# Kernel tuning notes

Measured on AMD Instinct MI355X. Metric: run time of the kernel, lower is better.

## Reference

```python
import jax, jax.numpy as jnp
import numpy as np

N_NODES = 50000


def _gcn_conv(x, W, b, src, dst, n_nodes):
    """PyG GCNConv: add self-loops, D^-1/2 (A+I) D^-1/2 X W + b."""
    loop = jnp.arange(n_nodes, dtype=src.dtype)
    src_f = jnp.concatenate([src, loop])  # [E+N]
    dst_f = jnp.concatenate([dst, loop])
    # degree over destination nodes (edge weight 1, incl. self loops)
    deg = jax.ops.segment_sum(jnp.ones_like(dst_f, dtype=x.dtype), dst_f,
                              num_segments=n_nodes)
    dinv = jnp.where(deg > 0, jax.lax.rsqrt(deg), 0.0)
    norm = dinv[src_f] * dinv[dst_f]  # [E+N]
    h = x @ W  # [N, C_out] dense GEMM first (C_out <= C_in here)
    msg = h[src_f] * norm[:, None]  # gather + scale
    out = jax.ops.segment_sum(msg, dst_f, num_segments=n_nodes)
    return out + b


def setup_inputs() -> dict:
    key = jax.random.key(0)
    k1, k2, k3, k4, k5, k6 = jax.random.split(key, 6)
    in_c, hid_c, out_c = 512, 512, 40
    x = jax.random.normal(k1, (N_NODES, in_c), dtype=jnp.float32)
    edge_index = jax.random.randint(k2, (2, 800000), 0, N_NODES, dtype=jnp.int64)
    # Glorot-style init for the linear weights, zero bias (PyG default)
    W1 = jax.random.normal(k3, (in_c, hid_c), dtype=jnp.float32) / np.sqrt(in_c)
    b1 = jnp.zeros((hid_c,), dtype=jnp.float32)
    W2 = jax.random.normal(k4, (hid_c, out_c), dtype=jnp.float32) / np.sqrt(hid_c)
    b2 = jnp.zeros((out_c,), dtype=jnp.float32)
    return {"x": x, "edge_index": edge_index, "W1": W1, "b1": b1,
            "W2": W2, "b2": b2}


def reference(x, edge_index, W1, b1, W2, b2):
    src, dst = edge_index[0], edge_index[1]
    h = _gcn_conv(x, W1, b1, src, dst, N_NODES)
    h = jax.nn.relu(h)
    h = _gcn_conv(h, W2, b2, src, dst, N_NODES)
    return jax.nn.log_softmax(h, axis=1)
```

## Files before the change

### kernel.cpp

```cpp
#include <hip/hip_runtime.h>


typedef unsigned int u32;
typedef unsigned short u16;
typedef __bf16 bf16x8 __attribute__((ext_vector_type(8)));
typedef float f32x4 __attribute__((ext_vector_type(4)));
typedef u32 u32x4 __attribute__((ext_vector_type(4)));

#define C_IN 512
#define C_HID 512
#define C_OUT 40
#define H_SCALE 24.0f
#define H_INV_SCALE (1.0f / 24.0f)

__device__ __forceinline__ float bf2f(u16 u) {
    u32 x = ((u32)u) << 16;
    return __builtin_bit_cast(float, x);
}
__device__ __forceinline__ u16 f2bf(float f) {
    u32 x = __builtin_bit_cast(u32, f);
    x += 0x7fffu + ((x >> 16) & 1u);
    return (u16)(x >> 16);
}
__device__ __forceinline__ char q8(float v) {
    float c = fminf(fmaxf(v * H_SCALE, -127.f), 127.f);
    return (char)__float2int_rn(c);
}
__device__ __forceinline__ u32 pk2(float a, float b) {
    u16 lo = __builtin_bit_cast(u16, (__bf16)a);
    u16 hi = __builtin_bit_cast(u16, (__bf16)b);
    return (u32)lo | ((u32)hi << 16);
}
__device__ __forceinline__ u32x4 pk8(float4 a, float4 b) {
    u32x4 r;
    r.x = pk2(a.x, a.y); r.y = pk2(a.z, a.w);
    r.z = pk2(b.x, b.y); r.w = pk2(b.z, b.w);
    return r;
}
__host__ __device__ __forceinline__ int imin(int a, int b) { return a < b ? a : b; }
__host__ __device__ __forceinline__ int imax(int a, int b) { return a > b ? a : b; }

__global__ void k_init(const u32* __restrict__ x32, const int* __restrict__ ei,
                       int* flags, int* deg, int* cursor, int n) {
    if (blockIdx.x == 0 && threadIdx.x < 64) {
        int lane = threadIdx.x;
        int z = (ei[2 * lane + 1] == 0) ? 1 : 0;
        u32 e = (x32[lane] >> 7) & 0xff;
        int v = (e >= 110 && e <= 133) ? 1 : 0;
        unsigned long long bz = __ballot(z);
        unsigned long long bv = __ballot(v);
        if (lane == 0) {
            flags[0] = (__popcll(bz) == 64) ? 2 : 1;
            flags[1] = (__popcll(bv) >= 48) ? 1 : 0;
        }
    }
    int i = blockIdx.x * 256 + threadIdx.x;
    if (i < n) { deg[i] = 1; cursor[i] = 0; }
}

__global__ void k_deg(const int* __restrict__ ei, const int* __restrict__ flags,
                      int* deg, int E, int ecap, int n) {
    int e = blockIdx.x * 256 + threadIdx.x;
    if (e >= E) return;
    int st = flags[0];
    int cap = ecap * st - 1;
    u32 d = (u32)ei[imin((E + e) * st, cap)];
    if (d < (u32)n) atomicAdd(&deg[d], 1);
}

__global__ void k_scanA(const int* __restrict__ deg, int* bsum, float* dinv, int n) {
    __shared__ int sh[256];
    int i = blockIdx.x * 256 + threadIdx.x;
    int dv = (i < n) ? deg[i] : 1;
    if (i < n) dinv[i] = rsqrtf((float)imax(dv, 1));
    sh[threadIdx.x] = (i < n) ? dv - 1 : 0;
    __syncthreads();
    for (int d = 128; d > 0; d >>= 1) {
        if (threadIdx.x < d) sh[threadIdx.x] += sh[threadIdx.x + d];
        __syncthreads();
    }
    if (threadIdx.x == 0) bsum[blockIdx.x] = sh[0];
}

__global__ void k_scanB(int* bsum, int nb, int* offs, int n) {
    __shared__ int sh[256];
    int t = threadIdx.x;
    int carry = 0;
    for (int base = 0; base < nb; base += 256) {
        int i = base + t;
        int v = (i < nb) ? bsum[i] : 0;
        sh[t] = v;
        __syncthreads();
        for (int d = 1; d < 256; d <<= 1) {
            int add = (t >= d) ? sh[t - d] : 0;
            __syncthreads();
            sh[t] += add;
            __syncthreads();
        }
        if (i < nb) bsum[i] = carry + sh[t] - v;
        int tot = sh[255];
        __syncthreads();
        carry += tot;
    }
    if (t == 0) offs[n] = carry;
}

__global__ void k_scanC(const int* __restrict__ deg, const int* __restrict__ bsum,
                        int* offs, int n) {
    __shared__ int sh[256];
    int t = threadIdx.x;
    int i = blockIdx.x * 256 + t;
    int v = (i < n) ? deg[i] - 1 : 0;
    sh[t] = v;
    __syncthreads();
    for (int d = 1; d < 256; d <<= 1) {
        int add = (t >= d) ? sh[t - d] : 0;
        __syncthreads();
        sh[t] += add;
        __syncthreads();
    }
    if (i < n) offs[i] = bsum[blockIdx.x] + sh[t] - v;
}

__global__ void k_sort(const int* __restrict__ ei, const int* __restrict__ flags,
                       const int* __restrict__ offs, int* cursor, int* csr,
                       int E, int ecap, int n) {
    int e = blockIdx.x * 256 + threadIdx.x;
    if (e >= E) return;
    int st = flags[0];
    int cap = ecap * st - 1;
    u32 d = (u32)ei[imin((E + e) * st, cap)];
    u32 s = (u32)ei[imin(e * st, cap)];
    if (d < (u32)n && s < (u32)n) {
        int pos = offs[d] + atomicAdd(&cursor[(int)d], 1);
        if ((u32)pos < (u32)E) csr[pos] = (int)s;
    }
}

__device__ __forceinline__ float ldf(const void* p, int i, int isbf) {
    return isbf ? bf2f(((const u16*)p)[i]) : ((const float*)p)[i];
}

__global__ __launch_bounds__(256) void k_prep(
    const void* __restrict__ W1, const void* __restrict__ b1,
    const void* __restrict__ W2, const void* __restrict__ b2,
    const int* __restrict__ flags, u16* __restrict__ w1t, u16* __restrict__ w2t,
    float* __restrict__ b1f, float* __restrict__ b2f) {
    __shared__ float tile[64][65];
    int isbf = flags[1];
    int tid = threadIdx.x;
    int stride = gridDim.x * 256;
    int i0 = blockIdx.x * 256 + tid;
    for (int t = blockIdx.x; t < 64; t += gridDim.x) {
        int tr = t >> 3, tc = t & 7;
        int rr = tid >> 2, cq = (tid & 3) * 16;
#pragma unroll
        for (int c = 0; c < 16; ++c)
            tile[cq + c][rr] = ldf(W1, (tr * 64 + rr) * 512 + tc * 64 + cq + c, isbf);
        __syncthreads();
#pragma unroll
        for (int c = 0; c < 16; ++c)
            w1t[(size_t)(tc * 64 + rr) * 512 + tr * 64 + cq + c] = f2bf(tile[rr][cq + c]);
        __syncthreads();
    }
    for (int i = i0; i < 64 * 512; i += stride) {
        int n = i >> 9, k = i & 511;
        w2t[i] = (n < C_OUT) ? f2bf(ldf(W2, k * C_OUT + n, isbf)) : (u16)0;
    }
    if (i0 < C_HID) b1f[i0] = ldf(b1, i0, isbf);
    if (i0 < C_OUT) b2f[i0] = ldf(b2, i0, isbf);
}

typedef __attribute__((address_space(1))) const u32 glds_src;
typedef __attribute__((address_space(3))) u32 glds_dst;

__global__ __launch_bounds__(256) void k_gemm128(
    const u16* __restrict__ xbf, const float* __restrict__ xf32,
    const int* __restrict__ flags, const u16* __restrict__ Bt,
    char* __restrict__ C, int M, int K, int ldc) {
    int isbf = flags[1];
    __shared__ __align__(16) u16 As0[64 * 32], As1[64 * 32];
    __shared__ __align__(16) u16 Bs0[128 * 32], Bs1[128 * 32];
    int tid = threadIdx.x;
    int wave = tid >> 6, lane = tid & 63;
    int quad = lane >> 4, lrow = lane & 15;
    int wrow = (wave & 1) * 32, wcol = (wave >> 1) * 64;

    int nwg = gridDim.x;
    int id = blockIdx.x;
    int q = nwg >> 3, r = nwg & 7;
    int xcd = id & 7, j8 = id >> 3;
    int wg = (xcd < r ? xcd * (q + 1) : r * (q + 1) + (xcd - r) * q) + j8;
    int row0 = (wg >> 2) * 64;
    int n0 = (wg & 3) * 128;

    int lr = lane >> 2;
    int lc = (lane & 3) * 8;
    int ar = row0 + wave * 16 + lr;
    int br = n0 + wave * 32 + lr;
    u16* As0_w = As0 + (wave * 16) * 32;
    u16* As1_w = As1 + (wave * 16) * 32;
    u16* Bs0_w = Bs0 + (wave * 32) * 32;
    u16* Bs1_w = Bs1 + (wave * 32) * 32;

    f32x4 acc[2][4] = {};
    int kTiles = K >> 6;
    for (int kt = 0; kt < kTiles; ++kt) {
        int k0 = kt * 64;
        int a0 = imin(ar, M - 1);
        if (isbf) {
            const u16* gA0 = xbf + (size_t)a0 * K + k0 + lc;
            __builtin_amdgcn_global_load_lds((glds_src*)gA0, (glds_dst*)As0_w, 16, 0, 0);
            __builtin_amdgcn_global_load_lds((glds_src*)(gA0 + 32), (glds_dst*)As1_w, 16, 0, 0);
        } else {
            const float* f0 = xf32 + (size_t)a0 * K + k0 + lc;
            float4 u0 = *(const float4*)(f0);
            float4 u1 = *(const float4*)(f0 + 4);
            float4 u2 = *(const float4*)(f0 + 32);
            float4 u3 = *(const float4*)(f0 + 36);
            *(u32x4*)(As0_w + lr * 32 + lc) = pk8(u0, u1);
            *(u32x4*)(As1_w + lr * 32 + lc) = pk8(u2, u3);
        }
        const u16* gB0 = Bt + (size_t)br * K + k0 + lc;
        const u16* gB1 = Bt + (size_t)(br + 16) * K + k0 + lc;
        __builtin_amdgcn_global_load_lds((glds_src*)gB0, (glds_dst*)Bs0_w, 16, 0, 0);
        __builtin_amdgcn_global_load_lds((glds_src*)gB1, (glds_dst*)(Bs0_w + 16 * 32), 16, 0, 0);
        __builtin_amdgcn_global_load_lds((glds_src*)(gB0 + 32), (glds_dst*)Bs1_w, 16, 0, 0);
        __builtin_amdgcn_global_load_lds((glds_src*)(gB1 + 32), (glds_dst*)(Bs1_w + 16 * 32), 16, 0, 0);
        __syncthreads();
#pragma unroll
        for (int ko = 0; ko < 2; ++ko) {
            const u16* Asrc = ko ? As1 : As0;
            const u16* Bsrc = ko ? Bs1 : Bs0;
            bf16x8 af[2], bfr[4];
#pragma unroll
            for (int i = 0; i < 2; ++i)
                af[i] = *(const bf16x8*)(Asrc + (wrow + i * 16 + lrow) * 32 + quad * 8);
#pragma unroll
            for (int j = 0; j < 4; ++j)
                bfr[j] = *(const bf16x8*)(Bsrc + (wcol + j * 16 + lrow) * 32 + quad * 8);
#pragma unroll
            for (int i = 0; i < 2; ++i)
#pragma unroll
                for (int j = 0; j < 4; ++j)
                    acc[i][j] = __builtin_amdgcn_mfma_f32_16x16x32_bf16(af[i], bfr[j],
                                                                        acc[i][j], 0, 0, 0);
        }
        __syncthreads();
    }
#pragma unroll
    for (int i = 0; i < 2; ++i)
#pragma unroll
        for (int j = 0; j < 4; ++j)
#pragma unroll
            for (int r2 = 0; r2 < 4; ++r2) {
                int row = row0 + wrow + i * 16 + quad * 4 + r2;
                int col = n0 + wcol + j * 16 + lrow;
                if (row < M) C[(size_t)row * ldc + col] = q8(acc[i][j][r2]);
            }
}

#define B2ROW 520
__global__ __launch_bounds__(256) void k_gemm64(
    const u16* __restrict__ A, const u16* __restrict__ Bt, u16* __restrict__ Cout,
    int M, int K, int Ncols, int ldc) {
    __shared__ __align__(16) u16 Bsh[48 * B2ROW];
    int tid = threadIdx.x;
    int wave = tid >> 6, lane = tid & 63;
    int quad = lane >> 4, lrow = lane & 15;

    for (int i = tid; i < 48 * 64; i += 256) {
        int rw = i >> 6, cv = (i & 63) * 8;
        *(uint4*)(Bsh + rw * B2ROW + cv) = *(const uint4*)(Bt + (size_t)rw * 512 + cv);
    }
    __syncthreads();

    int row0 = blockIdx.x * 128 + wave * 32;
    int r0 = imin(row0 + lrow, M - 1);
    int r1 = imin(row0 + 16 + lrow, M - 1);
    const u16* a0p = A + (size_t)r0 * K + quad * 8;
    const u16* a1p = A + (size_t)r1 * K + quad * 8;
    const u16* b0p = Bsh + (0 * 16 + lrow) * B2ROW + quad * 8;
    const u16* b1p = Bsh + (1 * 16 + lrow) * B2ROW + quad * 8;
    const u16* b2p = Bsh + (2 * 16 + lrow) * B2ROW + quad * 8;

    f32x4 c00 = {}, c01 = {}, c02 = {};
    f32x4 c10 = {}, c11 = {}, c12 = {};
#pragma unroll 4
    for (int k0 = 0; k0 < C_HID; k0 += 32) {
        bf16x8 a0 = *(const bf16x8*)(a0p + k0);
        bf16x8 a1 = *(const bf16x8*)(a1p + k0);
        bf16x8 b0 = *(const bf16x8*)(b0p + k0);
        bf16x8 b1 = *(const bf16x8*)(b1p + k0);
        bf16x8 b2 = *(const bf16x8*)(b2p + k0);
        c00 = __builtin_amdgcn_mfma_f32_16x16x32_bf16(a0, b0, c00, 0, 0, 0);
        c01 = __builtin_amdgcn_mfma_f32_16x16x32_bf16(a0, b1, c01, 0, 0, 0);
        c02 = __builtin_amdgcn_mfma_f32_16x16x32_bf16(a0, b2, c02, 0, 0, 0);
        c10 = __builtin_amdgcn_mfma_f32_16x16x32_bf16(a1, b0, c10, 0, 0, 0);
        c11 = __builtin_amdgcn_mfma_f32_16x16x32_bf16(a1, b1, c11, 0, 0, 0);
        c12 = __builtin_amdgcn_mfma_f32_16x16x32_bf16(a1, b2, c12, 0, 0, 0);
    }
    f32x4 cc[2][3] = {{c00, c01, c02}, {c10, c11, c12}};
#pragma unroll
    for (int i = 0; i < 2; ++i)
#pragma unroll
        for (int t = 0; t < 3; ++t)
#pragma unroll
            for (int r = 0; r < 4; ++r) {
                int row = row0 + i * 16 + quad * 4 + r;
                int col = t * 16 + lrow;
                if (row < M && col < Ncols)
                    Cout[(size_t)row * ldc + col] = f2bf(cc[i][t][r]);
            }
}

__device__ __forceinline__ void accum8i(float* acc, uint2 p, float w) {
    int lo = (int)p.x, hi = (int)p.y;
    acc[0] += w * (float)(signed char)(lo);
    acc[1] += w * (float)(signed char)(lo >> 8);
    acc[2] += w * (float)(signed char)(lo >> 16);
    acc[3] += w * (float)(signed char)(lo >> 24);
    acc[4] += w * (float)(signed char)(hi);
    acc[5] += w * (float)(signed char)(hi >> 8);
    acc[6] += w * (float)(signed char)(hi >> 16);
    acc[7] += w * (float)(signed char)(hi >> 24);
}

__global__ __launch_bounds__(256) void k_agg1(
    const char* __restrict__ hq, const int* __restrict__ csr, const int* __restrict__ offs,
    const float* __restrict__ dinv, const float* __restrict__ b1f,
    u16* __restrict__ out, int n, int Etot) {
    int wave = threadIdx.x >> 6, lane = threadIdx.x & 63;
    int v = blockIdx.x * 4 + wave;
    if (v >= n) return;
    float dv = dinv[v];
    float wself = dv * dv * H_INV_SCALE;

    float acc[8] = {0.f, 0.f, 0.f, 0.f, 0.f, 0.f, 0.f, 0.f};
    uint2 hs = *(const uint2*)(hq + (size_t)v * C_HID + lane * 8);
    accum8i(acc, hs, wself);

    int e0 = imax(0, imin(offs[v], Etot));
    int e1 = imax(e0, imin(offs[v + 1], Etot));
    for (int base = e0; base < e1; base += 64) {
        int cnt = imin(64, e1 - base);
        int sreg = 0; float wreg = 0.f;
        if (lane < cnt) {
            u32 s = (u32)csr[base + lane];
            s = (s < (u32)n) ? s : 0u;
            sreg = (int)s;
            wreg = dv * dinv[s] * H_INV_SCALE;
        }
        int j = 0;
        for (; j + 16 <= cnt; j += 16) {
            int ss[16]; float ww[16]; uint2 pp[16];
#pragma unroll
            for (int t = 0; t < 16; ++t) {
                ss[t] = __shfl(sreg, j + t);
                ww[t] = __shfl(wreg, j + t);
            }
#pragma unroll
            for (int t = 0; t < 16; ++t)
                pp[t] = *(const uint2*)(hq + (size_t)ss[t] * C_HID + lane * 8);
#pragma unroll
            for (int t = 0; t < 16; ++t) accum8i(acc, pp[t], ww[t]);
        }
        for (; j + 8 <= cnt; j += 8) {
            int ss[8]; float ww[8]; uint2 pp[8];
#pragma unroll
            for (int t = 0; t < 8; ++t) {
                ss[t] = __shfl(sreg, j + t);
                ww[t] = __shfl(wreg, j + t);
            }
#pragma unroll
            for (int t = 0; t < 8; ++t)
                pp[t] = *(const uint2*)(hq + (size_t)ss[t] * C_HID + lane * 8);
#pragma unroll
            for (int t = 0; t < 8; ++t) accum8i(acc, pp[t], ww[t]);
        }
        for (; j + 4 <= cnt; j += 4) {
            int ss[4]; float ww[4]; uint2 pp[4];
#pragma unroll
            for (int t = 0; t < 4; ++t) {
                ss[t] = __shfl(sreg, j + t);
                ww[t] = __shfl(wreg, j + t);
            }
#pragma unroll
            for (int t = 0; t < 4; ++t)
                pp[t] = *(const uint2*)(hq + (size_t)ss[t] * C_HID + lane * 8);
#pragma unroll
            for (int t = 0; t < 4; ++t) accum8i(acc, pp[t], ww[t]);
        }
        for (; j < cnt; ++j) {
            int sj = __shfl(sreg, j);
            float wj = __shfl(wreg, j);
            uint2 pj = *(const uint2*)(hq + (size_t)sj * C_HID + lane * 8);
            accum8i(acc, pj, wj);
        }
    }

    float4 ba = *(const float4*)(b1f + lane * 8);
    float4 bb = *(const float4*)(b1f + lane * 8 + 4);
    float r0 = fmaxf(acc[0] + ba.x, 0.f), r1 = fmaxf(acc[1] + ba.y, 0.f);
    float r2 = fmaxf(acc[2] + ba.z, 0.f), r3 = fmaxf(acc[3] + ba.w, 0.f);
    float r4 = fmaxf(acc[4] + bb.x, 0.f), r5 = fmaxf(acc[5] + bb.y, 0.f);
    float r6 = fmaxf(acc[6] + bb.z, 0.f), r7 = fmaxf(acc[7] + bb.w, 0.f);
    u32x4 o;
    o.x = (u32)f2bf(r0) | ((u32)f2bf(r1) << 16);
    o.y = (u32)f2bf(r2) | ((u32)f2bf(r3) << 16);
    o.z = (u32)f2bf(r4) | ((u32)f2bf(r5) << 16);
    o.w = (u32)f2bf(r6) | ((u32)f2bf(r7) << 16);
    __builtin_nontemporal_store(o, (u32x4*)(out + (size_t)v * C_HID + lane * 8));
}

__global__ __launch_bounds__(256) void k_agg2(
    const u16* __restrict__ h2, const int* __restrict__ csr, const int* __restrict__ offs,
    const float* __restrict__ dinv, const float* __restrict__ b2f,
    const int* __restrict__ flags, void* __restrict__ out, int n, int Etot) {
    int wave = threadIdx.x >> 6, lane = threadIdx.x & 63;
    int v = blockIdx.x * 4 + wave;
    if (v >= n) return;
    float dv = dinv[v];

    int g = lane / 10;
    int f4 = lane - g * 10;
    bool active = (g < 6);

    float4 acc = make_float4(0.f, 0.f, 0.f, 0.f);
    if (g == 0) {
        uint2 pv = *(const uint2*)(h2 + (size_t)v * C_OUT + f4 * 4);
        float w = dv * dv;
        acc.x = w * bf2f((u16)pv.x); acc.y = w * bf2f((u16)(pv.x >> 16));
        acc.z = w * bf2f((u16)pv.y); acc.w = w * bf2f((u16)(pv.y >> 16));
    }

    int e0 = imax(0, imin(offs[v], Etot));
    int e1 = imax(e0, imin(offs[v + 1], Etot));
    for (int base = e0; base < e1; base += 64) {
        int cnt = imin(64, e1 - base);
        int sreg = 0; float wreg = 0.f;
        if (lane < cnt) {
            u32 s = (u32)csr[base + lane];
            s = (s < (u32)n) ? s : 0u;
            sreg = (int)s;
            wreg = dv * dinv[s];
        }
        for (int j = 0; j < cnt; j += 24) {
            uint2 p[4]; float w4[4];
#pragma unroll
            for (int t = 0; t < 4; ++t) {
                int jj = j + t * 6 + g;
                int idx = imin(jj, cnt - 1);
                int sj = __shfl(sreg, idx);
                float wj = __shfl(wreg, idx);
                w4[t] = (active && jj < cnt) ? wj : 0.f;
                p[t] = make_uint2(0, 0);
                if (active) p[t] = *(const uint2*)(h2 + (size_t)sj * C_OUT + f4 * 4);
            }
#pragma unroll
            for (int t = 0; t < 4; ++t) {
                acc.x += w4[t] * bf2f((u16)p[t].x);
                acc.y += w4[t] * bf2f((u16)(p[t].x >> 16));
                acc.z += w4[t] * bf2f((u16)p[t].y);
                acc.w += w4[t] * bf2f((u16)(p[t].y >> 16));
            }
        }
    }

    float4 t;
    t.x = __shfl(acc.x, lane + 30); t.y = __shfl(acc.y, lane + 30);
    t.z = __shfl(acc.z, lane + 30); t.w = __shfl(acc.w, lane + 30);
    if (lane < 30) { acc.x += t.x; acc.y += t.y; acc.z += t.z; acc.w += t.w; }
    float4 t1, t2;
    t1.x = __shfl(acc.x, lane + 10); t1.y = __shfl(acc.y, lane + 10);
    t1.z = __shfl(acc.z, lane + 10); t1.w = __shfl(acc.w, lane + 10);
    t2.x = __shfl(acc.x, lane + 20); t2.y = __shfl(acc.y, lane + 20);
    t2.z = __shfl(acc.z, lane + 20); t2.w = __shfl(acc.w, lane + 20);
    if (lane < 10) {
        acc.x += t1.x + t2.x; acc.y += t1.y + t2.y;
        acc.z += t1.z + t2.z; acc.w += t1.w + t2.w;
        acc.x += b2f[f4 * 4 + 0]; acc.y += b2f[f4 * 4 + 1];
        acc.z += b2f[f4 * 4 + 2]; acc.w += b2f[f4 * 4 + 3];
    }

    float m = -1e30f;
    if (lane < 10) m = fmaxf(fmaxf(acc.x, acc.y), fmaxf(acc.z, acc.w));
    for (int off = 32; off > 0; off >>= 1) m = fmaxf(m, __shfl_xor(m, off));
    float s = 0.f;
    if (lane < 10)
        s = expf(acc.x - m) + expf(acc.y - m) + expf(acc.z - m) + expf(acc.w - m);
    for (int off = 32; off > 0; off >>= 1) s += __shfl_xor(s, off);
    if (lane < 10) {
        float ls = m + logf(s);
        if (flags[1]) {
            ushort4 o;
            o.x = f2bf(acc.x - ls); o.y = f2bf(acc.y - ls);
            o.z = f2bf(acc.z - ls); o.w = f2bf(acc.w - ls);
            *(ushort4*)((u16*)out + (size_t)v * C_OUT + f4 * 4) = o;
        } else {
            float4 o = make_float4(acc.x - ls, acc.y - ls, acc.z - ls, acc.w - ls);
            *(float4*)((float*)out + (size_t)v * C_OUT + f4 * 4) = o;
        }
    }
}


extern "C" void kernel_launch(void* const* d_in, const int* in_sizes, int n_in,
                              void* d_out, int out_size, void* d_ws, size_t ws_size,
                              hipStream_t stream) {
    const void* x = d_in[0];
    const int* ei = (const int*)d_in[1];
    const void* W1 = d_in[2];
    const void* b1 = d_in[3];
    const void* W2 = d_in[4];
    const void* b2 = d_in[5];

    const int N = out_size / C_OUT;
    const int Mx = in_sizes[0] / C_IN;
    const int M = (N < Mx) ? N : Mx;
    const int ECAP = in_sizes[1];
    const int E = ECAP / 2;

    char* p = (char*)d_ws;
    size_t used = 0;
    auto carve = [&](size_t bytes) -> void* {
        void* r = (void*)p;
        size_t b = (bytes + 255) & ~(size_t)255;
        p += b; used += b;
        return r;
    };
    int* flags = (int*)carve(256);
    int* deg = (int*)carve((size_t)N * 4);
    int* cursor = (int*)carve((size_t)N * 4);
    float* dinv = (float*)carve((size_t)N * 4);
    int* offs = (int*)carve((size_t)(N + 1) * 4);
    int* bsum = (int*)carve(8192);
    int* csr = (int*)carve((size_t)E * 4);
    u16* w1t = (u16*)carve((size_t)C_HID * C_IN * 2);
    u16* w2t = (u16*)carve((size_t)64 * C_HID * 2);
    float* b1f = (float*)carve(C_HID * 4);
    float* b2f = (float*)carve(256);
    u16* bufA = (u16*)carve((size_t)N * C_HID * 2);
    u16* bufB = (u16*)carve((size_t)N * C_HID * 2);
    if (used > ws_size) return;

    char* h_i8 = (char*)bufB;
    u16* hagg = bufA;
    u16* h2 = bufB;

    const int NB = (N + 255) / 256;
    const int EB = (E + 255) / 256;

    k_init<<<NB, 256, 0, stream>>>((const u32*)x, ei, flags, deg, cursor, N);
    k_deg<<<EB, 256, 0, stream>>>(ei, flags, deg, E, ECAP, N);
    k_scanA<<<NB, 256, 0, stream>>>(deg, bsum, dinv, N);
    k_scanB<<<1, 256, 0, stream>>>(bsum, NB, offs, N);
    k_scanC<<<NB, 256, 0, stream>>>(deg, bsum, offs, N);
    k_sort<<<EB, 256, 0, stream>>>(ei, flags, offs, cursor, csr, E, ECAP, N);

    k_prep<<<256, 256, 0, stream>>>(W1, b1, W2, b2, flags, w1t, w2t, b1f, b2f);

    int nbx = (M + 63) / 64;
    k_gemm128<<<nbx * 4, 256, 0, stream>>>((const u16*)x, (const float*)x, flags,
                                           w1t, h_i8, M, C_IN, C_HID);

    k_agg1<<<(N + 3) / 4, 256, 0, stream>>>(h_i8, csr, offs, dinv, b1f, hagg, N, E);

    k_gemm64<<<(M + 127) / 128, 256, 0, stream>>>(hagg, w2t, h2, N, C_HID, C_OUT, C_OUT);

    k_agg2<<<(N + 3) / 4, 256, 0, stream>>>(h2, csr, offs, dinv, b2f, flags, d_out, N, E);
}
```

Before: 404.5 us.

## Fuse init with weight prep and replace three-pass scan with decoupled look-back

Merges the init kernel with the weight transpose/convert prep kernel, so every block computes the format flags locally in shared memory. It also replaces the three-kernel offset scan (block sums, single-block scan, add-back) with one kernel that uses a decoupled look-back over a per-chunk state array. The aim is to cut kernel launches and serial gaps in the preprocessing chain. The look-back spins on prior blocks, so it relies on earlier blocks being scheduled first, and every block now redundantly recomputes the flag ballots.

Result: no change. 399.0 us (-1.4%).

```diff
diff --git a/kernel.cpp b/kernel.cpp
--- a/kernel.cpp
+++ b/kernel.cpp
@@ -3,6 +3,7 @@
 
 typedef unsigned int u32;
 typedef unsigned short u16;
+typedef unsigned long long u64;
 typedef __bf16 bf16x8 __attribute__((ext_vector_type(8)));
 typedef float f32x4 __attribute__((ext_vector_type(4)));
 typedef u32 u32x4 __attribute__((ext_vector_type(4)));
@@ -40,22 +41,58 @@
 __host__ __device__ __forceinline__ int imin(int a, int b) { return a < b ? a : b; }
 __host__ __device__ __forceinline__ int imax(int a, int b) { return a > b ? a : b; }
 
-__global__ void k_init(const u32* __restrict__ x32, const int* __restrict__ ei,
-                       int* flags, int* deg, int* cursor, int n) {
-    if (blockIdx.x == 0 && threadIdx.x < 64) {
-        int lane = threadIdx.x;
+__device__ __forceinline__ float ldf(const void* p, int i, int isbf) {
+    return isbf ? bf2f(((const u16*)p)[i]) : ((const float*)p)[i];
+}
+
+__global__ __launch_bounds__(256) void k_initprep(
+    const u32* __restrict__ x32, const int* __restrict__ ei,
+    const void* __restrict__ W1, const void* __restrict__ b1,
+    const void* __restrict__ W2, const void* __restrict__ b2,
+    int* flags, int* deg, int* cursor, u64* state,
+    u16* __restrict__ w1t, u16* __restrict__ w2t,
+    float* __restrict__ b1f, float* __restrict__ b2f,
+    int n, int nchunks) {
+    __shared__ float tile[64][65];
+    __shared__ int s_flags[2];
+    int tid = threadIdx.x;
+    if (tid < 64) {
+        int lane = tid;
         int z = (ei[2 * lane + 1] == 0) ? 1 : 0;
         u32 e = (x32[lane] >> 7) & 0xff;
         int v = (e >= 110 && e <= 133) ? 1 : 0;
         unsigned long long bz = __ballot(z);
         unsigned long long bv = __ballot(v);
         if (lane == 0) {
-            flags[0] = (__popcll(bz) == 64) ? 2 : 1;
-            flags[1] = (__popcll(bv) >= 48) ? 1 : 0;
-        }
-    }
-    int i = blockIdx.x * 256 + threadIdx.x;
-    if (i < n) { deg[i] = 1; cursor[i] = 0; }
+            s_flags[0] = (__popcll(bz) == 64) ? 2 : 1;
+            s_flags[1] = (__popcll(bv) >= 48) ? 1 : 0;
+        }
+    }
+    __syncthreads();
+    int isbf = s_flags[1];
+    int i0 = blockIdx.x * 256 + tid;
+    int stride = gridDim.x * 256;
+    if (blockIdx.x == 0 && tid == 0) { flags[0] = s_flags[0]; flags[1] = isbf; }
+    if (i0 < n) { deg[i0] = 1; cursor[i0] = 0; }
+    if (i0 < nchunks) state[i0] = 0ULL;
+    if (blockIdx.x < 64) {
+        int t = blockIdx.x;
+        int tr = t >> 3, tc = t & 7;
+        int rr = tid >> 2, cq = (tid & 3) * 16;
+#pragma unroll
+        for (int c = 0; c < 16; ++c)
+            tile[cq + c][rr] = ldf(W1, (tr * 64 + rr) * 512 + tc * 64 + cq + c, isbf);
+        __syncthreads();
+#pragma unroll
+        for (int c = 0; c < 16; ++c)
+            w1t[(size_t)(tc * 64 + rr) * 512 + tr * 64 + cq + c] = f2bf(tile[rr][cq + c]);
+    }
+    for (int i = i0; i < 64 * 512; i += stride) {
+        int nn = i >> 9, k = i & 511;
+        w2t[i] = (nn < C_OUT) ? f2bf(ldf(W2, k * C_OUT + nn, isbf)) : (u16)0;
+    }
+    if (i0 < C_HID) b1f[i0] = ldf(b1, i0, isbf);
+    if (i0 < C_OUT) b2f[i0] = ldf(b2, i0, isbf);
 }
 
 __global__ void k_deg(const int* __restrict__ ei, const int* __restrict__ flags,
@@ -68,58 +105,44 @@
     if (d < (u32)n) atomicAdd(&deg[d], 1);
 }
 
-__global__ void k_scanA(const int* __restrict__ deg, int* bsum, float* dinv, int n) {
+__global__ __launch_bounds__(256) void k_scan(
+    const int* __restrict__ deg, float* __restrict__ dinv, int* __restrict__ offs,
+    u64* state, int n, int nchunks) {
     __shared__ int sh[256];
-    int i = blockIdx.x * 256 + threadIdx.x;
+    __shared__ int s_prefix;
+    int tid = threadIdx.x;
+    int c = blockIdx.x;
+    int i = c * 256 + tid;
     int dv = (i < n) ? deg[i] : 1;
     if (i < n) dinv[i] = rsqrtf((float)imax(dv, 1));
-    sh[threadIdx.x] = (i < n) ? dv - 1 : 0;
-    __syncthreads();
-    for (int d = 128; d > 0; d >>= 1) {
-        if (threadIdx.x < d) sh[threadIdx.x] += sh[threadIdx.x + d];
-        __syncthreads();
-    }
-    if (threadIdx.x == 0) bsum[blockIdx.x] = sh[0];
-}
-
-__global__ void k_scanB(int* bsum, int nb, int* offs, int n) {
-    __shared__ int sh[256];
-    int t = threadIdx.x;
-    int carry = 0;
-    for (int base = 0; base < nb; base += 256) {
-        int i = base + t;
-        int v = (i < nb) ? bsum[i] : 0;
-        sh[t] = v;
-        __syncthreads();
-        for (int d = 1; d < 256; d <<= 1) {
-            int add = (t >= d) ? sh[t - d] : 0;
-            __syncthreads();
-            sh[t] += add;
-            __syncthreads();
-        }
-        if (i < nb) bsum[i] = carry + sh[t] - v;
-        int tot = sh[255];
-        __syncthreads();
-        carry += tot;
-    }
-    if (t == 0) offs[n] = carry;
-}
-
-__global__ void k_scanC(const int* __restrict__ deg, const int* __restrict__ bsum,
-                        int* offs, int n) {
-    __shared__ int sh[256];
-    int t = threadIdx.x;
-    int i = blockIdx.x * 256 + t;
-    int v = (i < n) ? deg[i] - 1 : 0;
-    sh[t] = v;
+    int v = (i < n) ? dv - 1 : 0;
+    sh[tid] = v;
     __syncthreads();
     for (int d = 1; d < 256; d <<= 1) {
-        int add = (t >= d) ? sh[t - d] : 0;
+        int add = (tid >= d) ? sh[tid - d] : 0;
         __syncthreads();
-        sh[t] += add;
+        sh[tid] += add;
         __syncthreads();
     }
-    if (i < n) offs[i] = bsum[blockIdx.x] + sh[t] - v;
+    int total = sh[255];
+    if (tid == 0) {
+        atomicExch(&state[c], (1ULL << 62) | (u64)(u32)total);
+        long long prefix = 0;
+        int cc = c - 1;
+        while (cc >= 0) {
+            u64 s;
+            do { s = atomicAdd(&state[cc], 0ULL); } while (s == 0ULL);
+            prefix += (long long)(u32)s;
+            if (s >> 63) break;
+            --cc;
+        }
+        atomicExch(&state[c], (1ULL << 63) | (u64)(u32)(prefix + total));
+        s_prefix = (int)prefix;
+        if (c == nchunks - 1) offs[n] = (int)(prefix + total);
+    }
+    __syncthreads();
+    int pfx = s_prefix;
+    if (i < n) offs[i] = pfx + sh[tid] - v;
 }
 
 __global__ void k_sort(const int* __restrict__ ei, const int* __restrict__ flags,
@@ -135,40 +158,6 @@
         int pos = offs[d] + atomicAdd(&cursor[(int)d], 1);
         if ((u32)pos < (u32)E) csr[pos] = (int)s;
     }
-}
-
-__device__ __forceinline__ float ldf(const void* p, int i, int isbf) {
-    return isbf ? bf2f(((const u16*)p)[i]) : ((const float*)p)[i];
-}
-
-__global__ __launch_bounds__(256) void k_prep(
-    const void* __restrict__ W1, const void* __restrict__ b1,
-    const void* __restrict__ W2, const void* __restrict__ b2,
-    const int* __restrict__ flags, u16* __restrict__ w1t, u16* __restrict__ w2t,
-    float* __restrict__ b1f, float* __restrict__ b2f) {
-    __shared__ float tile[64][65];
-    int isbf = flags[1];
-    int tid = threadIdx.x;
-    int stride = gridDim.x * 256;
-    int i0 = blockIdx.x * 256 + tid;
-    for (int t = blockIdx.x; t < 64; t += gridDim.x) {
-        int tr = t >> 3, tc = t & 7;
-        int rr = tid >> 2, cq = (tid & 3) * 16;
-#pragma unroll
-        for (int c = 0; c < 16; ++c)
-            tile[cq + c][rr] = ldf(W1, (tr * 64 + rr) * 512 + tc * 64 + cq + c, isbf);
-        __syncthreads();
-#pragma unroll
-        for (int c = 0; c < 16; ++c)
-            w1t[(size_t)(tc * 64 + rr) * 512 + tr * 64 + cq + c] = f2bf(tile[rr][cq + c]);
-        __syncthreads();
-    }
-    for (int i = i0; i < 64 * 512; i += stride) {
-        int n = i >> 9, k = i & 511;
-        w2t[i] = (n < C_OUT) ? f2bf(ldf(W2, k * C_OUT + n, isbf)) : (u16)0;
-    }
-    if (i0 < C_HID) b1f[i0] = ldf(b1, i0, isbf);
-    if (i0 < C_OUT) b2f[i0] = ldf(b2, i0, isbf);
 }
 
 typedef __attribute__((address_space(1))) const u32 glds_src;
@@ -534,7 +523,7 @@
     int* cursor = (int*)carve((size_t)N * 4);
     float* dinv = (float*)carve((size_t)N * 4);
     int* offs = (int*)carve((size_t)(N + 1) * 4);
-    int* bsum = (int*)carve(8192);
+    u64* state = (u64*)carve(4096);
     int* csr = (int*)carve((size_t)E * 4);
     u16* w1t = (u16*)carve((size_t)C_HID * C_IN * 2);
     u16* w2t = (u16*)carve((size_t)64 * C_HID * 2);
@@ -551,14 +540,12 @@
     const int NB = (N + 255) / 256;
     const int EB = (E + 255) / 256;
 
-    k_init<<<NB, 256, 0, stream>>>((const u32*)x, ei, flags, deg, cursor, N);
+    k_initprep<<<NB, 256, 0, stream>>>((const u32*)x, ei, W1, b1, W2, b2,
+                                       flags, deg, cursor, state,
+                                       w1t, w2t, b1f, b2f, N, NB);
     k_deg<<<EB, 256, 0, stream>>>(ei, flags, deg, E, ECAP, N);
-    k_scanA<<<NB, 256, 0, stream>>>(deg, bsum, dinv, N);
-    k_scanB<<<1, 256, 0, stream>>>(bsum, NB, offs, N);
-    k_scanC<<<NB, 256, 0, stream>>>(deg, bsum, offs, N);
+    k_scan<<<NB, 256, 0, stream>>>(deg, dinv, offs, state, N, NB);
     k_sort<<<EB, 256, 0, stream>>>(ei, flags, offs, cursor, csr, E, ECAP, N);
-
-    k_prep<<<256, 256, 0, stream>>>(W1, b1, W2, b2, flags, w1t, w2t, b1f, b2f);
 
     int nbx = (M + 63) / 64;
     k_gemm128<<<nbx * 4, 256, 0, stream>>>((const u16*)x, (const float*)x, flags,
```
